# Optimization experiments

Hardware: AMD Instinct MI355X
Metric: run time of the kernel (lower is better)

## Reference

```python
import jax, jax.numpy as jnp
import numpy as np
from jax import lax

NUM_STEPS = 32
NUM_CLASSES = 10
HIDDEN = 1024


def setup_inputs() -> dict:
    key = jax.random.key(0)
    ks = jax.random.split(key, 4)
    B, H, W, C = 8, 1024, 2048, 4
    x = jax.random.normal(ks[0], (B, H, W, C), dtype=jnp.float32)
    conv_w = jax.random.normal(ks[1], (C,), dtype=jnp.float32) * 0.5
    conv_b = jnp.zeros((1,), dtype=jnp.float32)
    w1 = jax.random.normal(ks[2], (HIDDEN, W), dtype=jnp.float32) * (1.0 / np.sqrt(W))
    b1 = jnp.zeros((HIDDEN,), dtype=jnp.float32)
    w2 = jax.random.normal(ks[3], (NUM_CLASSES, HIDDEN), dtype=jnp.float32) * (1.0 / np.sqrt(HIDDEN))
    b2 = jnp.zeros((NUM_CLASSES,), dtype=jnp.float32)
    beta1 = jnp.full((1,), 0.95, dtype=jnp.float32)
    thr1 = jnp.ones((1,), dtype=jnp.float32)
    beta2 = jnp.full((1,), 0.95, dtype=jnp.float32)
    thr2 = jnp.ones((1,), dtype=jnp.float32)
    return {"x": x, "conv_w": conv_w, "conv_b": conv_b, "w1": w1, "b1": b1,
            "beta1": beta1, "thr1": thr1, "w2": w2, "b2": b2,
            "beta2": beta2, "thr2": thr2}


def _leaky_scan(inp_t, beta, thr):
    # inp_t: [T, ...]; snntorch Leaky, reset_mechanism='subtract', reset_delay=False
    b = jnp.clip(beta, 0.0, 1.0)

    def step(mem, u):
        mem = b * mem + u
        spk = (mem > thr).astype(u.dtype)   # heaviside spike
        mem = mem - spk * thr               # subtract reset (no delay)
        return mem, spk

    mem0 = jnp.zeros(inp_t.shape[1:], dtype=inp_t.dtype)
    _, spks = lax.scan(step, mem0, inp_t)
    return spks  # [T, ...]


def reference(x, conv_w, conv_b, w1, b1, beta1, thr1, w2, b2, beta2, thr2):
    # x: [B, H, W, 4]; 1x1 conv over 4 antenna channels -> 1 channel
    xf = jnp.einsum('bhwc,c->bhw', x, conv_w) + conv_b[0]       # [B, H, W]
    B, H, W = xf.shape
    G = H // NUM_STEPS
    xr = xf.reshape(B, G, NUM_STEPS, W)                          # [B, G, T, 2048]
    h = jnp.einsum('bgtw,dw->bgtd', xr, w1) + b1                 # [B, G, T, D]
    spks1 = _leaky_scan(jnp.moveaxis(h, 2, 0), beta1, thr1)      # [T, B, G, D]
    s = spks1.sum(axis=0)                                        # [B, G, D]
    h2 = jnp.einsum('bgd,cd->bgc', s, w2) + b2                   # [B, G, C]
    spks2 = _leaky_scan(jnp.moveaxis(h2, 1, 0), beta2, thr2)     # [G, B, C]
    logits = spks2.sum(axis=0)                                   # [B, C]
    return jax.nn.softmax(logits, axis=1)
```

## Files before the change

kernel.cpp:

```cpp
#include <hip/hip_runtime.h>

#define TSTEPS 32
#define HID 1024
#define NCLS 10
#define BATCH 8
#define GGRP 32
#define MROWS 8192
#define GK 2048
#define GN 1024

typedef __attribute__((ext_vector_type(8))) short bf16x8;
typedef __attribute__((ext_vector_type(16))) float f32x16;

__device__ __forceinline__ unsigned short bf16_rne(float v) {
    unsigned u = __builtin_bit_cast(unsigned, v);
    return (unsigned short)((u + 0x7FFFu + ((u >> 16) & 1u)) >> 16);
}
__device__ __forceinline__ float bf16_f(unsigned short h) {
    unsigned u = (unsigned)h << 16;
    return __builtin_bit_cast(float, u);
}
__device__ __forceinline__ void gload16(const unsigned short* g, unsigned short* l) {
    __builtin_amdgcn_global_load_lds(
        (const __attribute__((address_space(1))) void*)g,
        (__attribute__((address_space(3))) void*)l, 16, 0, 0);
}


__global__ __launch_bounds__(256) void conv_pack_kernel(
    const float4* __restrict__ x, const float* __restrict__ cw,
    const float* __restrict__ cb,
    unsigned short* __restrict__ Ahi, unsigned short* __restrict__ Alo)
{
    const int rb = blockIdx.x >> 6;
    const int kb = blockIdx.x & 63;
    const float c0 = cw[0], c1 = cw[1], c2 = cw[2], c3 = cw[3], cbv = cb[0];
    const int tid = threadIdx.x;
#pragma unroll
    for (int cc = 0; cc < 2; ++cc) {
        int c = tid + cc * 256;
        int u = c >> 6, w = c & 63;
        int row = (u >> 1) * 32 + (w & 31);
        int k0  = (u & 1) * 16 + (w >> 5) * 8;
        const float4* px = x + ((size_t)(rb * 128 + row) * 2048 + kb * 32 + k0);
        bf16x8 h8, l8;
#pragma unroll
        for (int e = 0; e < 8; ++e) {
            float4 a = px[e];
            float v = a.x * c0 + a.y * c1 + a.z * c2 + a.w * c3 + cbv;
            unsigned short h = bf16_rne(v);
            h8[e] = (short)h;
            l8[e] = (short)bf16_rne(v - bf16_f(h));
        }
        size_t off = ((size_t)blockIdx.x * 512 + c) * 8;
        *(bf16x8*)(Ahi + off) = h8;
        *(bf16x8*)(Alo + off) = l8;
    }
}

__global__ __launch_bounds__(256) void wpack_kernel(
    const float* __restrict__ wsrc, unsigned short* __restrict__ Bhi,
    unsigned short* __restrict__ Blo)
{
    const int kb = blockIdx.x & 63;
    const int cbk = blockIdx.x >> 6;
    const int tid = threadIdx.x;
#pragma unroll
    for (int cc = 0; cc < 2; ++cc) {
        int c = tid + cc * 256;
        int u = c >> 6, w = c & 63;
        int row = (u >> 1) * 32 + (w & 31);
        int k0  = (u & 1) * 16 + (w >> 5) * 8;
        const float* pw = wsrc + ((size_t)(cbk * 128 + row) * 2048 + kb * 32 + k0);
        bf16x8 h8, l8;
#pragma unroll
        for (int e = 0; e < 8; ++e) {
            float v = pw[e];
            unsigned short h = bf16_rne(v);
            h8[e] = (short)h;
            l8[e] = (short)bf16_rne(v - bf16_f(h));
        }
        size_t off = ((size_t)blockIdx.x * 512 + c) * 8;
        *(bf16x8*)(Bhi + off) = h8;
        *(bf16x8*)(Blo + off) = l8;
    }
}

__global__ __launch_bounds__(256) void gemm_scan_kernel(
    const unsigned short* __restrict__ Ahi, const unsigned short* __restrict__ Alo,
    const unsigned short* __restrict__ Bhi, const unsigned short* __restrict__ Blo,
    const float* __restrict__ bias,
    const float* __restrict__ beta1, const float* __restrict__ thr1,
    float* __restrict__ S)
{
    __shared__ __align__(16) unsigned short smem[2][16384];

    const int tid = threadIdx.x;
    const int lane = tid & 63, wv = tid >> 6;
    const int wr = wv >> 1, wc = wv & 1;
    const int rb = blockIdx.y;
    const int col0 = blockIdx.x * 128;

    const unsigned short* gAh = Ahi + (size_t)rb * (64 * 4096);
    const unsigned short* gAl = Alo + (size_t)rb * (64 * 4096);
    const unsigned short* gBh = Bhi + (size_t)blockIdx.x * (64 * 4096);
    const unsigned short* gBl = Blo + (size_t)blockIdx.x * (64 * 4096);

    f32x16 acc[2][2];
#pragma unroll
    for (int i = 0; i < 2; ++i)
#pragma unroll
        for (int j = 0; j < 2; ++j) acc[i][j] = (f32x16)0.f;

#define STAGE(buf, kb_)                                                          \
    {                                                                            \
        const size_t tb = (size_t)(kb_) * 4096;                                  \
        unsigned short* dst = &smem[buf][0];                                     \
        _Pragma("unroll")                                                        \
        for (int ii = 0; ii < 2; ++ii) {                                         \
            size_t so = tb + (size_t)(wv * 128 + ii * 64 + lane) * 8;            \
            int dl = (wv * 128 + ii * 64) * 8;                                   \
            gload16(gAh + so, dst + 0 + dl);                                     \
            gload16(gAl + so, dst + 4096 + dl);                                  \
            gload16(gBh + so, dst + 8192 + dl);                                  \
            gload16(gBl + so, dst + 12288 + dl);                                 \
        }                                                                        \
    }

    STAGE(0, 0);
    __syncthreads();

    const int fo = ((lane & 31) + 32 * (lane >> 5)) * 8;

    int cur = 0;
    for (int kb = 0; kb < 64; ++kb) {
        if (kb < 63) STAGE(cur ^ 1, kb + 1);

        const unsigned short* bufp = &smem[cur][0];
        bf16x8 ah[2][2], al[2][2], bh[2][2], bl[2][2];
#pragma unroll
        for (int i = 0; i < 2; ++i)
#pragma unroll
            for (int kh = 0; kh < 2; ++kh) {
                int ua = (((wr * 2 + i) * 2 + kh) << 9) + fo;
                int ub = (((wc * 2 + i) * 2 + kh) << 9) + fo;
                ah[i][kh] = *(const bf16x8*)(bufp + 0 + ua);
                al[i][kh] = *(const bf16x8*)(bufp + 4096 + ua);
                bh[i][kh] = *(const bf16x8*)(bufp + 8192 + ub);
                bl[i][kh] = *(const bf16x8*)(bufp + 12288 + ub);
            }
#pragma unroll
        for (int kh = 0; kh < 2; ++kh) {
#pragma unroll
            for (int i = 0; i < 2; ++i)
#pragma unroll
                for (int j = 0; j < 2; ++j)
                    acc[i][j] = __builtin_amdgcn_mfma_f32_32x32x16_bf16(ah[i][kh], bh[j][kh], acc[i][j], 0, 0, 0);
#pragma unroll
            for (int i = 0; i < 2; ++i)
#pragma unroll
                for (int j = 0; j < 2; ++j)
                    acc[i][j] = __builtin_amdgcn_mfma_f32_32x32x16_bf16(ah[i][kh], bl[j][kh], acc[i][j], 0, 0, 0);
#pragma unroll
            for (int i = 0; i < 2; ++i)
#pragma unroll
                for (int j = 0; j < 2; ++j)
                    acc[i][j] = __builtin_amdgcn_mfma_f32_32x32x16_bf16(al[i][kh], bh[j][kh], acc[i][j], 0, 0, 0);
        }
        __syncthreads();
        cur ^= 1;
    }

    float* sb = (float*)&smem[0][0];
    const float bclamp = fminf(fmaxf(beta1[0], 0.f), 1.f);
    const float th = thr1[0];
    const int sbg = tid >> 7;
    const int scol = tid & 127;
    const float bv = bias[col0 + scol];

#pragma unroll
    for (int band = 0; band < 2; ++band) {
        if (wr == band) {
#pragma unroll
            for (int i = 0; i < 2; ++i)
#pragma unroll
                for (int j = 0; j < 2; ++j)
#pragma unroll
                    for (int r = 0; r < 16; ++r) {
                        int lr = i * 32 + (r & 3) + 8 * (r >> 2) + 4 * (lane >> 5);
                        int lc = wc * 64 + j * 32 + (lane & 31);
                        sb[lr * 132 + lc] = acc[i][j][r];
                    }
        }
        __syncthreads();
        float mem = 0.f, cnt = 0.f;
#pragma unroll
        for (int t = 0; t < TSTEPS; ++t) {
            float u = sb[(sbg * 32 + t) * 132 + scol] + bv;
            mem = bclamp * mem + u;
            float spk = mem > th ? 1.f : 0.f;
            mem -= spk * th;
            cnt += spk;
        }
        int bgg = ((rb * 128) >> 5) + band * 2 + sbg;
        S[(size_t)bgg * GN + col0 + scol] = cnt;
        __syncthreads();
    }
}

__global__ __launch_bounds__(256) void fc2_kernel(
    const float* __restrict__ s, const float* __restrict__ w2,
    const float* __restrict__ b2, float* __restrict__ h2)
{
    int bg  = blockIdx.x;
    int tid = threadIdx.x;
    const float* sp = s + (size_t)bg * HID;
    float part[NCLS];
#pragma unroll
    for (int c = 0; c < NCLS; ++c) part[c] = 0.f;
    for (int d = tid; d < HID; d += 256) {
        float sv = sp[d];
#pragma unroll
        for (int c = 0; c < NCLS; ++c) part[c] += sv * w2[c * HID + d];
    }
#pragma unroll
    for (int c = 0; c < NCLS; ++c)
        for (int off = 32; off > 0; off >>= 1)
            part[c] += __shfl_down(part[c], off, 64);
    __shared__ float red[NCLS][4];
    int wave = tid >> 6, lanei = tid & 63;
    if (lanei == 0)
#pragma unroll
        for (int c = 0; c < NCLS; ++c) red[c][wave] = part[c];
    __syncthreads();
    if (tid < NCLS) {
        float v = red[tid][0] + red[tid][1] + red[tid][2] + red[tid][3] + b2[tid];
        h2[bg * NCLS + tid] = v;
    }
}

__global__ __launch_bounds__(128) void scan2_kernel(
    const float* __restrict__ h2, const float* __restrict__ beta2,
    const float* __restrict__ thr2, float* __restrict__ out)
{
    __shared__ float logits[BATCH][NCLS];
    int t = threadIdx.x;
    if (t < BATCH * NCLS) {
        int b = t / NCLS, c = t % NCLS;
        float bb = fminf(fmaxf(beta2[0], 0.f), 1.f);
        float th = thr2[0];
        float mem = 0.f, lg = 0.f;
        for (int g = 0; g < GGRP; ++g) {
            float u = h2[(b * GGRP + g) * NCLS + c];
            mem = bb * mem + u;
            float spk = mem > th ? 1.f : 0.f;
            mem -= spk * th;
            lg += spk;
        }
        logits[b][c] = lg;
    }
    __syncthreads();
    if (t < BATCH) {
        float mx = -1e30f;
        for (int c = 0; c < NCLS; ++c) mx = fmaxf(mx, logits[t][c]);
        float e[NCLS];
        float sum = 0.f;
        for (int c = 0; c < NCLS; ++c) { e[c] = expf(logits[t][c] - mx); sum += e[c]; }
        for (int c = 0; c < NCLS; ++c) out[t * NCLS + c] = e[c] / sum;
    }
}

extern "C" void kernel_launch(void* const* d_in, const int* in_sizes, int n_in,
                              void* d_out, int out_size, void* d_ws, size_t ws_size,
                              hipStream_t stream)
{
    const float* x     = (const float*)d_in[0];
    const float* cw    = (const float*)d_in[1];
    const float* cb    = (const float*)d_in[2];
    const float* w1    = (const float*)d_in[3];
    const float* b1    = (const float*)d_in[4];
    const float* beta1 = (const float*)d_in[5];
    const float* thr1  = (const float*)d_in[6];
    const float* w2    = (const float*)d_in[7];
    const float* b2    = (const float*)d_in[8];
    const float* beta2 = (const float*)d_in[9];
    const float* thr2  = (const float*)d_in[10];
    float* out = (float*)d_out;

    unsigned short* ahi = (unsigned short*)d_ws;
    unsigned short* alo = ahi + (size_t)MROWS * GK;
    unsigned short* bhi = alo + (size_t)MROWS * GK;
    unsigned short* blo = bhi + (size_t)GN * GK;
    float* s  = (float*)(blo + (size_t)GN * GK);
    float* h2 = s + (size_t)BATCH * GGRP * HID;

    conv_pack_kernel<<<4096, 256, 0, stream>>>((const float4*)x, cw, cb, ahi, alo);
    wpack_kernel    <<<512, 256, 0, stream>>>(w1, bhi, blo);
    gemm_scan_kernel<<<dim3(8, 64), 256, 0, stream>>>(ahi, alo, bhi, blo, b1, beta1, thr1, s);
    fc2_kernel      <<<256, 256, 0, stream>>>(s, w2, b2, h2);
    scan2_kernel    <<<1, 128, 0, stream>>>(h2, beta2, thr2, out);
}
```

Measured before the change: 179.7 us.

## Widen GEMM tile to 128x256 with 8 waves and triple-buffered LDS pipeline

```diff
diff --git a/kernel.cpp b/kernel.cpp
--- a/kernel.cpp
+++ b/kernel.cpp
@@ -8,6 +8,7 @@
 #define MROWS 8192
 #define GK 2048
 #define GN 1024
+#define BUFSH 24576
 
 typedef __attribute__((ext_vector_type(8))) short bf16x8;
 typedef __attribute__((ext_vector_type(16))) float f32x16;
@@ -62,16 +63,16 @@
     const float* __restrict__ wsrc, unsigned short* __restrict__ Bhi,
     unsigned short* __restrict__ Blo)
 {
-    const int kb = blockIdx.x & 63;
+    const int kb  = blockIdx.x & 63;
     const int cbk = blockIdx.x >> 6;
     const int tid = threadIdx.x;
 #pragma unroll
-    for (int cc = 0; cc < 2; ++cc) {
+    for (int cc = 0; cc < 4; ++cc) {
         int c = tid + cc * 256;
         int u = c >> 6, w = c & 63;
-        int row = (u >> 1) * 32 + (w & 31);
-        int k0  = (u & 1) * 16 + (w >> 5) * 8;
-        const float* pw = wsrc + ((size_t)(cbk * 128 + row) * 2048 + kb * 32 + k0);
+        int col = cbk * 256 + (u >> 1) * 32 + (w & 31);
+        int k0  = kb * 32 + (u & 1) * 16 + (w >> 5) * 8;
+        const float* pw = wsrc + ((size_t)col * 2048 + k0);
         bf16x8 h8, l8;
 #pragma unroll
         for (int e = 0; e < 8; ++e) {
@@ -80,31 +81,31 @@
             h8[e] = (short)h;
             l8[e] = (short)bf16_rne(v - bf16_f(h));
         }
-        size_t off = ((size_t)blockIdx.x * 512 + c) * 8;
+        size_t off = ((size_t)blockIdx.x * 1024 + c) * 8;
         *(bf16x8*)(Bhi + off) = h8;
         *(bf16x8*)(Blo + off) = l8;
     }
 }
 
-__global__ __launch_bounds__(256) void gemm_scan_kernel(
+__global__ __launch_bounds__(512) void gemm_scan_kernel(
     const unsigned short* __restrict__ Ahi, const unsigned short* __restrict__ Alo,
     const unsigned short* __restrict__ Bhi, const unsigned short* __restrict__ Blo,
     const float* __restrict__ bias,
     const float* __restrict__ beta1, const float* __restrict__ thr1,
     float* __restrict__ S)
 {
-    __shared__ __align__(16) unsigned short smem[2][16384];
+    __shared__ __align__(16) unsigned short sm[3 * BUFSH];
 
     const int tid = threadIdx.x;
     const int lane = tid & 63, wv = tid >> 6;
-    const int wr = wv >> 1, wc = wv & 1;
-    const int rb = blockIdx.y;
-    const int col0 = blockIdx.x * 128;
-
-    const unsigned short* gAh = Ahi + (size_t)rb * (64 * 4096);
-    const unsigned short* gAl = Alo + (size_t)rb * (64 * 4096);
-    const unsigned short* gBh = Bhi + (size_t)blockIdx.x * (64 * 4096);
-    const unsigned short* gBl = Blo + (size_t)blockIdx.x * (64 * 4096);
+    const int wr = wv >> 2, wc = wv & 3;
+    const int by = blockIdx.x & 63;
+    const int bx = blockIdx.x >> 6;
+
+    const unsigned short* gAh = Ahi + (size_t)by * 262144;
+    const unsigned short* gAl = Alo + (size_t)by * 262144;
+    const unsigned short* gBh = Bhi + (size_t)bx * 524288;
+    const unsigned short* gBl = Blo + (size_t)bx * 524288;
 
     f32x16 acc[2][2];
 #pragma unroll
@@ -114,40 +115,48 @@
 
 #define STAGE(buf, kb_)                                                          \
     {                                                                            \
-        const size_t tb = (size_t)(kb_) * 4096;                                  \
-        unsigned short* dst = &smem[buf][0];                                     \
-        _Pragma("unroll")                                                        \
-        for (int ii = 0; ii < 2; ++ii) {                                         \
-            size_t so = tb + (size_t)(wv * 128 + ii * 64 + lane) * 8;            \
-            int dl = (wv * 128 + ii * 64) * 8;                                   \
-            gload16(gAh + so, dst + 0 + dl);                                     \
-            gload16(gAl + so, dst + 4096 + dl);                                  \
-            gload16(gBh + so, dst + 8192 + dl);                                  \
-            gload16(gBl + so, dst + 12288 + dl);                                 \
-        }                                                                        \
+        unsigned short* dst = sm + (buf) * BUFSH;                                \
+        const size_t ao = (size_t)(kb_) * 4096 + tid * 8;                        \
+        const size_t bo = (size_t)(kb_) * 8192 + tid * 8;                        \
+        gload16(gAh + ao, dst + tid * 8);                                        \
+        gload16(gAl + ao, dst + 4096 + tid * 8);                                 \
+        gload16(gBh + bo, dst + 8192 + tid * 8);                                 \
+        gload16(gBh + bo + 4096, dst + 12288 + tid * 8);                         \
+        gload16(gBl + bo, dst + 16384 + tid * 8);                                \
+        gload16(gBl + bo + 4096, dst + 20480 + tid * 8);                         \
     }
 
     STAGE(0, 0);
-    __syncthreads();
+    STAGE(1, 1);
 
     const int fo = ((lane & 31) + 32 * (lane >> 5)) * 8;
 
     int cur = 0;
     for (int kb = 0; kb < 64; ++kb) {
-        if (kb < 63) STAGE(cur ^ 1, kb + 1);
-
-        const unsigned short* bufp = &smem[cur][0];
+        if (kb < 63) asm volatile("s_waitcnt vmcnt(6)" ::: "memory");
+        else         asm volatile("s_waitcnt vmcnt(0)" ::: "memory");
+        __builtin_amdgcn_s_barrier();
+
+        int nbuf = cur + 2; if (nbuf >= 3) nbuf -= 3;
+        if (kb < 62) STAGE(nbuf, kb + 2);
+
+        const unsigned short* bufp = sm + cur * BUFSH;
         bf16x8 ah[2][2], al[2][2], bh[2][2], bl[2][2];
 #pragma unroll
         for (int i = 0; i < 2; ++i)
 #pragma unroll
             for (int kh = 0; kh < 2; ++kh) {
                 int ua = (((wr * 2 + i) * 2 + kh) << 9) + fo;
-                int ub = (((wc * 2 + i) * 2 + kh) << 9) + fo;
-                ah[i][kh] = *(const bf16x8*)(bufp + 0 + ua);
+                ah[i][kh] = *(const bf16x8*)(bufp + ua);
                 al[i][kh] = *(const bf16x8*)(bufp + 4096 + ua);
-                bh[i][kh] = *(const bf16x8*)(bufp + 8192 + ub);
-                bl[i][kh] = *(const bf16x8*)(bufp + 12288 + ub);
+            }
+#pragma unroll
+        for (int j = 0; j < 2; ++j)
+#pragma unroll
+            for (int kh = 0; kh < 2; ++kh) {
+                int ub = (((wc * 2 + j) * 2 + kh) << 9) + fo;
+                bh[j][kh] = *(const bf16x8*)(bufp + 8192 + ub);
+                bl[j][kh] = *(const bf16x8*)(bufp + 16384 + ub);
             }
 #pragma unroll
         for (int kh = 0; kh < 2; ++kh) {
@@ -167,16 +176,16 @@
                 for (int j = 0; j < 2; ++j)
                     acc[i][j] = __builtin_amdgcn_mfma_f32_32x32x16_bf16(al[i][kh], bh[j][kh], acc[i][j], 0, 0, 0);
         }
-        __syncthreads();
-        cur ^= 1;
-    }
-
-    float* sb = (float*)&smem[0][0];
+        cur = (cur == 2) ? 0 : cur + 1;
+    }
+    __syncthreads();
+
+    float* sb = (float*)sm;
     const float bclamp = fminf(fmaxf(beta1[0], 0.f), 1.f);
     const float th = thr1[0];
-    const int sbg = tid >> 7;
-    const int scol = tid & 127;
-    const float bv = bias[col0 + scol];
+    const int sbg = tid >> 8;
+    const int scol = tid & 255;
+    const float bv = bias[bx * 256 + scol];
 
 #pragma unroll
     for (int band = 0; band < 2; ++band) {
@@ -189,21 +198,21 @@
                     for (int r = 0; r < 16; ++r) {
                         int lr = i * 32 + (r & 3) + 8 * (r >> 2) + 4 * (lane >> 5);
                         int lc = wc * 64 + j * 32 + (lane & 31);
-                        sb[lr * 132 + lc] = acc[i][j][r];
+                        sb[lr * 256 + lc] = acc[i][j][r];
                     }
         }
         __syncthreads();
         float mem = 0.f, cnt = 0.f;
 #pragma unroll
         for (int t = 0; t < TSTEPS; ++t) {
-            float u = sb[(sbg * 32 + t) * 132 + scol] + bv;
+            float u = sb[(sbg * 32 + t) * 256 + scol] + bv;
             mem = bclamp * mem + u;
             float spk = mem > th ? 1.f : 0.f;
             mem -= spk * th;
             cnt += spk;
         }
-        int bgg = ((rb * 128) >> 5) + band * 2 + sbg;
-        S[(size_t)bgg * GN + col0 + scol] = cnt;
+        int bgg = by * 4 + band * 2 + sbg;
+        S[(size_t)bgg * GN + bx * 256 + scol] = cnt;
         __syncthreads();
     }
 }
@@ -295,8 +304,8 @@
     float* h2 = s + (size_t)BATCH * GGRP * HID;
 
     conv_pack_kernel<<<4096, 256, 0, stream>>>((const float4*)x, cw, cb, ahi, alo);
-    wpack_kernel    <<<512, 256, 0, stream>>>(w1, bhi, blo);
-    gemm_scan_kernel<<<dim3(8, 64), 256, 0, stream>>>(ahi, alo, bhi, blo, b1, beta1, thr1, s);
+    wpack_kernel    <<<256, 256, 0, stream>>>(w1, bhi, blo);
+    gemm_scan_kernel<<<256, 512, 0, stream>>>(ahi, alo, bhi, blo, b1, beta1, thr1, s);
     fc2_kernel      <<<256, 256, 0, stream>>>(s, w2, b2, h2);
     scan2_kernel    <<<1, 128, 0, stream>>>(h2, beta2, thr2, out);
 }
```

After: 171.6 us. -4.5%, faster.
